# Performance work log

Hardware: AMD Instinct MI355X
Metric: run time of the kernel (lower is better)

Reference implementation:

```python
import jax, jax.numpy as jnp
import numpy as np

NEG_SLOPE = 0.01  # nn.LeakyReLU default


def gcn_conv(x, src, dst, deg_inv_sqrt, W, b, n_nodes):
    """PyG GCNConv with self-loops already folded into (src, dst, deg_inv_sqrt).
    out = scatter_add(norm_e * (x @ W)[src]) + b, norm_e = d_src^-1/2 * d_dst^-1/2."""
    h = x @ W  # [N, F_out] -- transform first (F_out < F_in saves gather traffic)
    norm = (deg_inv_sqrt[src] * deg_inv_sqrt[dst])[:, None]  # [E, 1]
    msg = h[src] * norm  # [E, F_out]
    return jax.ops.segment_sum(msg, dst, num_segments=n_nodes) + b


def setup_inputs() -> dict:
    key = jax.random.key(0)
    ks = jax.random.split(key, 8)
    N, E, F_IN, F_HID, F_OUT = 50000, 800000, 256, 128, 64
    x = jax.random.normal(ks[0], (N, F_IN), dtype=jnp.float32)
    edge_index = jax.random.randint(ks[1], (2, E), 0, N, dtype=jnp.int64)
    def glorot(k, shape):
        lim = float(np.sqrt(6.0 / (shape[0] + shape[1])))
        return jax.random.uniform(k, shape, jnp.float32, -lim, lim)
    return {
        "x": x,
        "edge_index": edge_index,
        "W1": glorot(ks[2], (F_IN, F_HID)),
        "b1": jnp.zeros((F_HID,), jnp.float32),
        "W_mu": glorot(ks[3], (F_HID, F_OUT)),
        "b_mu": jnp.zeros((F_OUT,), jnp.float32),
        "W_logvar": glorot(ks[4], (F_HID, F_OUT)),
        "b_logvar": jnp.zeros((F_OUT,), jnp.float32),
    }


def reference(x, edge_index, W1, b1, W_mu, b_mu, W_logvar, b_logvar):
    n_nodes = x.shape[0]
    loops = jnp.arange(n_nodes, dtype=edge_index.dtype)
    src = jnp.concatenate([edge_index[0], loops])
    dst = jnp.concatenate([edge_index[1], loops])
    # degree on destination nodes (includes self-loop); >= 1 so rsqrt is safe
    deg = jax.ops.segment_sum(jnp.ones_like(dst, dtype=x.dtype), dst, num_segments=n_nodes)
    deg_inv_sqrt = jax.lax.rsqrt(deg)

    h = gcn_conv(x, src, dst, deg_inv_sqrt, W1, b1, n_nodes)
    h = jax.nn.leaky_relu(h, NEG_SLOPE)
    mu = gcn_conv(h, src, dst, deg_inv_sqrt, W_mu, b_mu, n_nodes)
    logvar = gcn_conv(h, src, dst, deg_inv_sqrt, W_logvar, b_logvar, n_nodes)
    return (mu, logvar)
```

## Files before the change

### kernel.cpp

```cpp
#include <hip/hip_runtime.h>

#define NEG_SLOPE 0.01f
#define EPB 4096
#define NB_SHIFT 8
#define PAD_SHIFT 13

typedef __attribute__((ext_vector_type(8))) short bf16x8;
typedef __attribute__((ext_vector_type(4))) float floatx4;

__device__ __forceinline__ short f2bf(float f) {
    union { float f; unsigned u; } v; v.f = f;
    unsigned u = v.u;
    u += 0x7FFF + ((u >> 16) & 1);
    return (short)(u >> 16);
}
__device__ __forceinline__ float bf2f(short s) {
    union { unsigned u; float f; } v;
    v.u = ((unsigned)(unsigned short)s) << 16;
    return v.f;
}

__launch_bounds__(256)
__global__ void pack_weights(const float* __restrict__ W1, const float* __restrict__ Wmu,
                             const float* __restrict__ Wlv,
                             short* __restrict__ w1f, short* __restrict__ wcatf,
                             int* __restrict__ bcur, int K) {
    if (blockIdx.x == 192) {
        if (threadIdx.x < K) bcur[threadIdx.x] = 0;
        return;
    }
    int i = blockIdx.x * 256 + threadIdx.x;
    if (i < 128 * 256) {
        int j  = i & 7;
        int ln = (i >> 3) & 15;
        int q  = (i >> 7) & 3;
        int t  = (i >> 9) & 7;
        int kb = i >> 12;
        int n = t * 16 + ln;
        int k = kb * 32 + q * 8 + j;
        w1f[i] = f2bf(W1[k * 128 + n]);
    } else {
        int i2 = i - 128 * 256;
        int j  = i2 & 7;
        int ln = (i2 >> 3) & 15;
        int q  = (i2 >> 7) & 3;
        int t  = (i2 >> 9) & 7;
        int kb = i2 >> 12;
        int n = t * 16 + ln;
        int k = kb * 32 + q * 8 + j;
        wcatf[i2] = f2bf((n < 64) ? Wmu[k * 64 + n] : Wlv[k * 64 + (n - 64)]);
    }
}

__device__ __forceinline__ void gemm1_body64(int blk, int tid, const float* __restrict__ Ap,
                                             const short* __restrict__ Bfrag,
                                             short* __restrict__ C, int M) {
    int w = tid >> 6;
    int lane = tid & 63;
    int ln = lane & 15;
    int q  = lane >> 4;
    int row0 = blk * 64 + w * 16;

    int r0 = row0 + ln;
    int r0c = (r0 < M) ? r0 : (M - 1);
    const float* aF = Ap + (size_t)r0c * 256 + q * 8;
    const short* bLane = Bfrag + lane * 8;

    floatx4 acc[8];
    #pragma unroll
    for (int t = 0; t < 8; t++) acc[t] = (floatx4){0.f, 0.f, 0.f, 0.f};

    #pragma unroll
    for (int kb = 0; kb < 8; kb++) {
        int kt = kb * 32;
        float4 x0 = *(const float4*)(aF + kt);
        float4 x1 = *(const float4*)(aF + kt + 4);
        bf16x8 a;
        a[0] = f2bf(x0.x); a[1] = f2bf(x0.y); a[2] = f2bf(x0.z); a[3] = f2bf(x0.w);
        a[4] = f2bf(x1.x); a[5] = f2bf(x1.y); a[6] = f2bf(x1.z); a[7] = f2bf(x1.w);
        bf16x8 bF[8];
        #pragma unroll
        for (int t = 0; t < 8; t++)
            bF[t] = *(const bf16x8*)(bLane + (size_t)(kb * 8 + t) * 512);
        #pragma unroll
        for (int t = 0; t < 8; t++)
            acc[t] = __builtin_amdgcn_mfma_f32_16x16x32_bf16(a, bF[t], acc[t], 0, 0, 0);
    }

    #pragma unroll
    for (int reg = 0; reg < 4; reg++) {
        int r = row0 + q * 4 + reg;
        if (r < M) {
            #pragma unroll
            for (int t = 0; t < 8; t++)
                C[(size_t)r * 128 + t * 16 + ln] = f2bf(acc[t][reg]);
        }
    }
}

__launch_bounds__(256)
__global__ void scatter_gemm1(const int* __restrict__ src, const int* __restrict__ dst,
                              int E, int B, int G64, int* __restrict__ bcur,
                              unsigned* __restrict__ bucketed,
                              const float* __restrict__ x, const short* __restrict__ w1f,
                              short* __restrict__ z1, int M) {
    __shared__ int lh[256];
    __shared__ int lofs[256];
    __shared__ int gbase[256];
    __shared__ unsigned srt[EPB];
    __shared__ int waveTot[4];
    __shared__ int waveOff[4];
    int bid = blockIdx.x;
    int tid = threadIdx.x;
    if (bid < G64) {
        gemm1_body64(bid, tid, x, w1f, z1, M);
    } else {
        int sbid = bid - G64;
        lh[tid] = 0;
        __syncthreads();
        int lo = sbid * EPB, hi = min(lo + EPB, E);
        for (int e = lo + tid; e < hi; e += 256)
            atomicAdd(&lh[dst[e] >> NB_SHIFT], 1);
        __syncthreads();
        int v = lh[tid];
        int lane = tid & 63, wave = tid >> 6;
        int s = v;
        #pragma unroll
        for (int o = 1; o < 64; o <<= 1) {
            int t = __shfl_up(s, o);
            if (lane >= o) s += t;
        }
        if (lane == 63) waveTot[wave] = s;
        __syncthreads();
        if (tid == 0) {
            int acc = 0;
            #pragma unroll
            for (int w = 0; w < 4; w++) { waveOff[w] = acc; acc += waveTot[w]; }
        }
        __syncthreads();
        int excl = s - v + waveOff[wave];
        lofs[tid] = excl;
        if (v) gbase[tid] = (tid << PAD_SHIFT) + atomicAdd(&bcur[tid], v);
        __syncthreads();
        lh[tid] = excl;
        __syncthreads();
        for (int e = lo + tid; e < hi; e += 256) {
            int d = dst[e];
            unsigned rec = (unsigned)(src[e] & 0xFFFF) | ((unsigned)d << 16);
            int p = atomicAdd(&lh[d >> NB_SHIFT], 1);
            srt[p] = rec;
        }
        __syncthreads();
        int cnt = hi - lo;
        for (int p = tid; p < cnt; p += 256) {
            unsigned r = srt[p];
            int k = r >> 24;
            int pos = gbase[k] + (p - lofs[k]);
            if (pos < ((k + 1) << PAD_SHIFT))
                bucketed[pos] = r;
        }
    }
}

__global__ void fill_csr_deg(const unsigned* __restrict__ bucketed,
                             const int* __restrict__ bcur,
                             int* __restrict__ row_ptr, int* __restrict__ row_end,
                             float* __restrict__ dis,
                             unsigned short* __restrict__ csr_src, int N) {
    __shared__ int cnt[256];
    __shared__ int rp[256];
    __shared__ int waveTot[4];
    __shared__ int waveOff[4];
    __shared__ unsigned short lcsr[8192];
    int k = blockIdx.x;
    int tid = threadIdx.x;
    int base = k << NB_SHIFT;
    cnt[tid] = 0;
    __syncthreads();
    int lo = k << PAD_SHIFT;
    int m = bcur[k];
    if (m > 8192) m = 8192;
    int hi = lo + m;
    for (int e = lo + tid; e < hi; e += 256)
        atomicAdd(&cnt[(bucketed[e] >> 16) & 255], 1);
    __syncthreads();
    int v = cnt[tid];
    int lane = tid & 63, wave = tid >> 6;
    int s = v;
    #pragma unroll
    for (int o = 1; o < 64; o <<= 1) {
        int t = __shfl_up(s, o);
        if (lane >= o) s += t;
    }
    if (lane == 63) waveTot[wave] = s;
    __syncthreads();
    if (tid == 0) {
        int acc = 0;
        #pragma unroll
        for (int w = 0; w < 4; w++) { waveOff[w] = acc; acc += waveTot[w]; }
    }
    __syncthreads();
    int excl = s - v + waveOff[wave];
    rp[tid] = excl;
    int node = base + tid;
    if (node < N) {
        row_ptr[node] = lo + excl;
        row_end[node] = lo + excl + v;
        dis[node] = rsqrtf(1.0f + (float)v);
    }
    __syncthreads();
    for (int e = lo + tid; e < hi; e += 256) {
        unsigned sd = bucketed[e];
        int p = atomicAdd(&rp[(sd >> 16) & 255], 1);
        lcsr[p] = (unsigned short)(sd & 0xFFFFu);
    }
    __syncthreads();
    for (int i = tid; i < m; i += 256) csr_src[lo + i] = lcsr[i];
}

template<bool WEIGHTED>
__device__ __forceinline__ void agg_quarter(const short* __restrict__ zb,
                                            const unsigned short* __restrict__ csr_src,
                                            const float* __restrict__ dis,
                                            int start, int end, int qbase, int fl,
                                            float acc[8]) {
    for (int bse = start; bse < end; bse += 16) {
        int n = end - bse; n = (n > 16) ? 16 : n;
        int idx = (int)csr_src[bse + ((fl < n) ? fl : 0)];
        float dl = WEIGHTED ? dis[idx] : 1.f;
        #pragma unroll
        for (int e = 0; e < 16; e += 8) {
            if (e >= n) break;
            bf16x8 r[8];
            float wt[8];
            #pragma unroll
            for (int k = 0; k < 8; ++k) {
                int ee = e + k;
                int s0 = __shfl(idx, qbase + ee);
                float we = WEIGHTED ? __shfl(dl, qbase + ee) : 1.f;
                wt[k] = (ee < n) ? we : 0.f;
                r[k] = *(const bf16x8*)(zb + (size_t)s0 * 128);
            }
            #pragma unroll
            for (int k = 0; k < 8; ++k)
                #pragma unroll
                for (int t = 0; t < 8; t++)
                    acc[t] = fmaf(wt[k], bf2f(r[k][t]), acc[t]);
        }
    }
}

__launch_bounds__(256)
__global__ void agg1_gemm2(const short* __restrict__ z1, const int* __restrict__ row_ptr,
                           const int* __restrict__ row_end,
                           const unsigned short* __restrict__ csr_src,
                           const float* __restrict__ dis, const float* __restrict__ b1,
                           const short* __restrict__ wcatf,
                           short* __restrict__ z2, int N) {
    __shared__ short htile[16 * 128];
    int tid = threadIdx.x;
    int w = tid >> 6;
    int lane = tid & 63;
    int qi = lane >> 4;
    int fl = lane & 15;
    int fo = fl * 8;
    int qbase = qi * 16;
    int base = blockIdx.x * 16;
    int local = w * 4 + qi;
    int node = base + local;

    short* hrow = &htile[(local * 128 + fo) ^ ((local & 7) * 8)];
    bf16x8 ov = (bf16x8){0, 0, 0, 0, 0, 0, 0, 0};
    if (node < N) {
        const short* zb = z1 + fo;
        int start = row_ptr[node], end = row_end[node];
        float acc[8];
        #pragma unroll
        for (int t = 0; t < 8; t++) acc[t] = 0.f;
        agg_quarter<true>(zb, csr_src, dis, start, end, qbase, fl, acc);
        float dn = dis[node];
        bf16x8 zs = *(const bf16x8*)(zb + (size_t)node * 128);
        #pragma unroll
        for (int t = 0; t < 8; t++) acc[t] = fmaf(dn, bf2f(zs[t]), acc[t]);
        #pragma unroll
        for (int t = 0; t < 8; t++) {
            float v = fmaf(dn, acc[t], b1[fo + t]);
            v = (v > 0.f) ? v : NEG_SLOPE * v;
            ov[t] = f2bf(v);
        }
    }
    *(bf16x8*)hrow = ov;
    __syncthreads();

    int r0 = fl;
    const short* bLane = wcatf + lane * 8;

    floatx4 acc[2];
    #pragma unroll
    for (int t = 0; t < 2; t++) acc[t] = (floatx4){0.f, 0.f, 0.f, 0.f};

    #pragma unroll
    for (int kb = 0; kb < 4; kb++) {
        int k0 = kb * 32 + qi * 8;
        bf16x8 aF = *(const bf16x8*)&htile[(r0 * 128 + k0) ^ ((r0 & 7) * 8)];
        #pragma unroll
        for (int t = 0; t < 2; t++) {
            int tt = w * 2 + t;
            bf16x8 bF = *(const bf16x8*)(bLane + (size_t)(kb * 8 + tt) * 512);
            acc[t] = __builtin_amdgcn_mfma_f32_16x16x32_bf16(aF, bF, acc[t], 0, 0, 0);
        }
    }

    #pragma unroll
    for (int reg = 0; reg < 4; reg++) {
        int gr = base + qi * 4 + reg;
        if (gr < N) {
            float s = dis[gr];
            #pragma unroll
            for (int t = 0; t < 2; t++)
                z2[(size_t)gr * 128 + (w * 2 + t) * 16 + fl] = f2bf(s * acc[t][reg]);
        }
    }
}

__launch_bounds__(256)
__global__ void agg_layer2(const short* __restrict__ zp, const int* __restrict__ row_ptr,
                           const int* __restrict__ row_end,
                           const unsigned short* __restrict__ csr_src,
                           const float* __restrict__ dis, const float* __restrict__ b_mu,
                           const float* __restrict__ b_lv, float* __restrict__ out, int N) {
    int tid = threadIdx.x;
    int w = tid >> 6;
    int lane = tid & 63;
    int qi = lane >> 4;
    int fl = lane & 15;
    int fo = fl * 8;
    int qbase = qi * 16;
    int node = blockIdx.x * 16 + w * 4 + qi;
    if (node >= N) return;

    const short* zb = zp + fo;
    int start = row_ptr[node], end = row_end[node];
    float acc[8];
    #pragma unroll
    for (int t = 0; t < 8; t++) acc[t] = 0.f;
    agg_quarter<false>(zb, csr_src, nullptr, start, end, qbase, fl, acc);
    bf16x8 zs = *(const bf16x8*)(zb + (size_t)node * 128);
    #pragma unroll
    for (int t = 0; t < 8; t++) acc[t] += bf2f(zs[t]);

    float d = dis[node];
    float r[8];
    if (fl < 8) {
        #pragma unroll
        for (int t = 0; t < 8; t++) r[t] = fmaf(d, acc[t], b_mu[fo + t]);
        float* p = out + (size_t)node * 64 + fo;
        *(float4*)p       = make_float4(r[0], r[1], r[2], r[3]);
        *(float4*)(p + 4) = make_float4(r[4], r[5], r[6], r[7]);
    } else {
        #pragma unroll
        for (int t = 0; t < 8; t++) r[t] = fmaf(d, acc[t], b_lv[fo - 64 + t]);
        float* p = out + (size_t)N * 64 + (size_t)node * 64 + (fo - 64);
        *(float4*)p       = make_float4(r[0], r[1], r[2], r[3]);
        *(float4*)(p + 4) = make_float4(r[4], r[5], r[6], r[7]);
    }
}


extern "C" void kernel_launch(void* const* d_in, const int* in_sizes, int n_in,
                              void* d_out, int out_size, void* d_ws, size_t ws_size,
                              hipStream_t stream) {
    const float* x   = (const float*)d_in[0];
    const int*   ei  = (const int*)d_in[1];
    const float* W1  = (const float*)d_in[2];
    const float* b1  = (const float*)d_in[3];
    const float* Wmu = (const float*)d_in[4];
    const float* bmu = (const float*)d_in[5];
    const float* Wlv = (const float*)d_in[6];
    const float* blv = (const float*)d_in[7];
    float* out = (float*)d_out;

    const int F_IN = 256;
    int N = in_sizes[0] / F_IN;
    int E = in_sizes[1] / 2;
    const int* e_src = ei;
    const int* e_dst = ei + E;

    int B = (E + EPB - 1) / EPB;
    int K = (N + 255) >> NB_SHIFT;
    int G64 = (N + 63) / 64;
    int G2 = (N + 15) / 16;

    char* ws = (char*)d_ws;
    size_t off = 0;
    auto carve = [&](size_t bytes) -> void* {
        void* p = ws + off;
        off += (bytes + 255) & ~(size_t)255;
        return p;
    };
    int*      row_end  = (int*)   carve((size_t)N * 4);
    int*      row_ptr  = (int*)   carve((size_t)N * 4);
    float*    dis      = (float*) carve((size_t)N * 4);
    unsigned short* csr_src = (unsigned short*)carve((size_t)K << PAD_SHIFT << 1);
    short*    bufA     = (short*) carve((size_t)N * 128 * 2);
    short*    bufB     = (short*) carve((size_t)N * 128 * 2);
    short*    w1f      = (short*) carve(128 * 256 * 2);
    short*    wcatf    = (short*) carve(128 * 128 * 2);
    int*      bcur     = (int*)   carve((size_t)K * 4);
    unsigned* bucketed = (unsigned*)carve((size_t)K << PAD_SHIFT << 2);

    hipLaunchKernelGGL(pack_weights, dim3(193), dim3(256), 0, stream,
                       W1, Wmu, Wlv, w1f, wcatf, bcur, K);
    hipLaunchKernelGGL(scatter_gemm1, dim3(G64 + B), dim3(256), 0, stream,
                       e_src, e_dst, E, B, G64, bcur, bucketed, x, w1f, bufA, N);
    hipLaunchKernelGGL(fill_csr_deg, dim3(K), dim3(256), 0, stream,
                       bucketed, bcur, row_ptr, row_end, dis, csr_src, N);
    hipLaunchKernelGGL(agg1_gemm2, dim3(G2), dim3(256), 0, stream,
                       bufA, row_ptr, row_end, csr_src, dis, b1, wcatf, bufB, N);
    hipLaunchKernelGGL(agg_layer2, dim3(G2), dim3(256), 0, stream,
                       bufB, row_ptr, row_end, csr_src, dis, bmu, blv, out, N);
}
```

Before: 195.5 us.

## Prefetch GEMM1 activations in halves, scope scatter LDS, widen CSR fill blocks

The GEMM1 body now issues all A-row loads for the first half of K up front, converts them to bf16, and prefetches the second half while the first half's MFMAs run. The goal is to hide global load latency. The scatter kernel's shared arrays are moved inside the scatter branch, which may not change LDS allocation. The CSR fill kernel now runs 512 threads per block, with the scan still done by the first 256, to raise memory-level parallelism when loading and storing bucket edges. The prefetch costs extra registers, which could lower occupancy.

```diff
diff --git a/kernel.cpp b/kernel.cpp
--- a/kernel.cpp
+++ b/kernel.cpp
@@ -70,21 +70,41 @@
     #pragma unroll
     for (int t = 0; t < 8; t++) acc[t] = (floatx4){0.f, 0.f, 0.f, 0.f};
 
-    #pragma unroll
-    for (int kb = 0; kb < 8; kb++) {
-        int kt = kb * 32;
-        float4 x0 = *(const float4*)(aF + kt);
-        float4 x1 = *(const float4*)(aF + kt + 4);
-        bf16x8 a;
-        a[0] = f2bf(x0.x); a[1] = f2bf(x0.y); a[2] = f2bf(x0.z); a[3] = f2bf(x0.w);
-        a[4] = f2bf(x1.x); a[5] = f2bf(x1.y); a[6] = f2bf(x1.z); a[7] = f2bf(x1.w);
-        bf16x8 bF[8];
-        #pragma unroll
-        for (int t = 0; t < 8; t++)
-            bF[t] = *(const bf16x8*)(bLane + (size_t)(kb * 8 + t) * 512);
-        #pragma unroll
-        for (int t = 0; t < 8; t++)
-            acc[t] = __builtin_amdgcn_mfma_f32_16x16x32_bf16(a, bF[t], acc[t], 0, 0, 0);
+    float4 a4[8];
+    #pragma unroll
+    for (int kb = 0; kb < 4; kb++) {
+        a4[kb * 2]     = *(const float4*)(aF + kb * 32);
+        a4[kb * 2 + 1] = *(const float4*)(aF + kb * 32 + 4);
+    }
+    #pragma unroll
+    for (int half = 0; half < 2; half++) {
+        bf16x8 aB[4];
+        #pragma unroll
+        for (int kb = 0; kb < 4; kb++) {
+            float4 x0 = a4[kb * 2], x1 = a4[kb * 2 + 1];
+            aB[kb][0] = f2bf(x0.x); aB[kb][1] = f2bf(x0.y);
+            aB[kb][2] = f2bf(x0.z); aB[kb][3] = f2bf(x0.w);
+            aB[kb][4] = f2bf(x1.x); aB[kb][5] = f2bf(x1.y);
+            aB[kb][6] = f2bf(x1.z); aB[kb][7] = f2bf(x1.w);
+        }
+        if (half == 0) {
+            #pragma unroll
+            for (int kb = 0; kb < 4; kb++) {
+                a4[kb * 2]     = *(const float4*)(aF + (kb + 4) * 32);
+                a4[kb * 2 + 1] = *(const float4*)(aF + (kb + 4) * 32 + 4);
+            }
+        }
+        #pragma unroll
+        for (int kb = 0; kb < 4; kb++) {
+            int kbg = half * 4 + kb;
+            bf16x8 bF[8];
+            #pragma unroll
+            for (int t = 0; t < 8; t++)
+                bF[t] = *(const bf16x8*)(bLane + (size_t)(kbg * 8 + t) * 512);
+            #pragma unroll
+            for (int t = 0; t < 8; t++)
+                acc[t] = __builtin_amdgcn_mfma_f32_16x16x32_bf16(aB[kb], bF[t], acc[t], 0, 0, 0);
+        }
     }
 
     #pragma unroll
@@ -104,17 +124,17 @@
                               unsigned* __restrict__ bucketed,
                               const float* __restrict__ x, const short* __restrict__ w1f,
                               short* __restrict__ z1, int M) {
-    __shared__ int lh[256];
-    __shared__ int lofs[256];
-    __shared__ int gbase[256];
-    __shared__ unsigned srt[EPB];
-    __shared__ int waveTot[4];
-    __shared__ int waveOff[4];
     int bid = blockIdx.x;
     int tid = threadIdx.x;
     if (bid < G64) {
         gemm1_body64(bid, tid, x, w1f, z1, M);
     } else {
+        __shared__ int lh[256];
+        __shared__ int lofs[256];
+        __shared__ int gbase[256];
+        __shared__ unsigned srt[EPB];
+        __shared__ int waveTot[4];
+        __shared__ int waveOff[4];
         int sbid = bid - G64;
         lh[tid] = 0;
         __syncthreads();
@@ -162,6 +182,7 @@
     }
 }
 
+__launch_bounds__(512)
 __global__ void fill_csr_deg(const unsigned* __restrict__ bucketed,
                              const int* __restrict__ bcur,
                              int* __restrict__ row_ptr, int* __restrict__ row_end,
@@ -175,24 +196,28 @@
     int k = blockIdx.x;
     int tid = threadIdx.x;
     int base = k << NB_SHIFT;
-    cnt[tid] = 0;
+    if (tid < 256) cnt[tid] = 0;
     __syncthreads();
     int lo = k << PAD_SHIFT;
     int m = bcur[k];
     if (m > 8192) m = 8192;
     int hi = lo + m;
-    for (int e = lo + tid; e < hi; e += 256)
+    for (int e = lo + tid; e < hi; e += 512)
         atomicAdd(&cnt[(bucketed[e] >> 16) & 255], 1);
     __syncthreads();
-    int v = cnt[tid];
     int lane = tid & 63, wave = tid >> 6;
-    int s = v;
-    #pragma unroll
-    for (int o = 1; o < 64; o <<= 1) {
-        int t = __shfl_up(s, o);
-        if (lane >= o) s += t;
-    }
-    if (lane == 63) waveTot[wave] = s;
+    int v = 0, excl = 0;
+    if (tid < 256) {
+        v = cnt[tid];
+        int s = v;
+        #pragma unroll
+        for (int o = 1; o < 64; o <<= 1) {
+            int t = __shfl_up(s, o);
+            if (lane >= o) s += t;
+        }
+        if (lane == 63) waveTot[wave] = s;
+        excl = s - v;
+    }
     __syncthreads();
     if (tid == 0) {
         int acc = 0;
@@ -200,22 +225,24 @@
         for (int w = 0; w < 4; w++) { waveOff[w] = acc; acc += waveTot[w]; }
     }
     __syncthreads();
-    int excl = s - v + waveOff[wave];
-    rp[tid] = excl;
-    int node = base + tid;
-    if (node < N) {
-        row_ptr[node] = lo + excl;
-        row_end[node] = lo + excl + v;
-        dis[node] = rsqrtf(1.0f + (float)v);
-    }
-    __syncthreads();
-    for (int e = lo + tid; e < hi; e += 256) {
+    if (tid < 256) {
+        excl += waveOff[wave];
+        rp[tid] = excl;
+        int node = base + tid;
+        if (node < N) {
+            row_ptr[node] = lo + excl;
+            row_end[node] = lo + excl + v;
+            dis[node] = rsqrtf(1.0f + (float)v);
+        }
+    }
+    __syncthreads();
+    for (int e = lo + tid; e < hi; e += 512) {
         unsigned sd = bucketed[e];
         int p = atomicAdd(&rp[(sd >> 16) & 255], 1);
         lcsr[p] = (unsigned short)(sd & 0xFFFFu);
     }
     __syncthreads();
-    for (int i = tid; i < m; i += 256) csr_src[lo + i] = lcsr[i];
+    for (int i = tid; i < m; i += 512) csr_src[lo + i] = lcsr[i];
 }
 
 template<bool WEIGHTED>
@@ -413,7 +440,7 @@
                        W1, Wmu, Wlv, w1f, wcatf, bcur, K);
     hipLaunchKernelGGL(scatter_gemm1, dim3(G64 + B), dim3(256), 0, stream,
                        e_src, e_dst, E, B, G64, bcur, bucketed, x, w1f, bufA, N);
-    hipLaunchKernelGGL(fill_csr_deg, dim3(K), dim3(256), 0, stream,
+    hipLaunchKernelGGL(fill_csr_deg, dim3(K), dim3(512), 0, stream,
                        bucketed, bcur, row_ptr, row_end, dis, csr_src, N);
     hipLaunchKernelGGL(agg1_gemm2, dim3(G2), dim3(256), 0, stream,
                        bufA, row_ptr, row_end, csr_src, dis, b1, wcatf, bufB, N);
```

Measured after the change: 193.7 us. No clear change (-0.9%).
